# Kernel optimization log

Measured on AMD Instinct MI355X. Metric: run time of the kernel, lower is better.

Reference implementation:

```python
import jax, jax.numpy as jnp
import numpy as np

NUM_CLASSES = 256
N_ITERS = 25  # fixed Lloyd iterations (sklearn default max_iter=300; fixed count for a jit-able reference)


def setup_inputs() -> dict:
    key = jax.random.key(0)
    k1, k2 = jax.random.split(key)
    features = jax.random.normal(k1, (65536, 1024), dtype=jnp.float32)
    logits = jax.random.normal(k2, (65536, 256), dtype=jnp.float32)
    return {"features": features, "logits": logits}


def _segment_mean_centroids(features, labels, num_classes, prev_centroids):
    # scatter-mean of features into per-class centroids; keep previous centroid if a class is empty
    sums = jax.ops.segment_sum(features, labels, num_segments=num_classes)      # [C, D]
    counts = jax.ops.segment_sum(jnp.ones((features.shape[0],), features.dtype),
                                 labels, num_segments=num_classes)               # [C]
    has = counts > 0
    means = sums / jnp.maximum(counts, 1.0)[:, None]
    return jnp.where(has[:, None], means, prev_centroids)


def _assign(features, centroids):
    # argmin of squared euclidean distance; ||x||^2 term is constant per row, drop it
    # scores[n, c] = -2 x_n . mu_c + ||mu_c||^2
    scores = -2.0 * jnp.einsum('nd,cd->nc', features, centroids) + jnp.sum(centroids * centroids, axis=1)[None, :]
    return jnp.argmin(scores, axis=1)


def reference(features, logits):
    # KMeans.forward: labels = argmax(logits); centroids init from label centers (centroid_init='label_centers');
    # then Lloyd's k-means (sklearn KMeans with init=centroids, n_init=1) and return cluster labels.
    init_labels = jnp.argmax(logits, axis=1)
    # get_centroids: empty classes stay at zero
    zeros = jnp.zeros((NUM_CLASSES, features.shape[1]), features.dtype)
    centroids = _segment_mean_centroids(features, init_labels, NUM_CLASSES, zeros)

    def body(i, centroids):
        labels = _assign(features, centroids)
        return _segment_mean_centroids(features, labels, NUM_CLASSES, centroids)

    centroids = jax.lax.fori_loop(0, N_ITERS, body, centroids)
    pseudo_labels = _assign(features, centroids)
    return pseudo_labels.astype(jnp.int64)
```

## Files before the change

### kernel.cpp

```cpp
#include <hip/hip_runtime.h>

#define N_PTS 65536
#define DIM   1024
#define NCLS  256
#define NITER 25

typedef __attribute__((ext_vector_type(8)))  short short8;
typedef __attribute__((ext_vector_type(16))) float f32x16;

__device__ __forceinline__ unsigned short bf_split(float x, float& rem) {
    unsigned u = __float_as_uint(x);
    unsigned b = (u + 0x7fffu + ((u >> 16) & 1u)) & 0xffff0000u;
    rem = x - __uint_as_float(b);
    return (unsigned short)(b >> 16);
}
__device__ __forceinline__ unsigned short bf_rne(float x) {
    unsigned u = __float_as_uint(x);
    return (unsigned short)((u + 0x7fffu + ((u >> 16) & 1u)) >> 16);
}

__device__ __forceinline__ void gload_lds16(const void* g, void* l) {
    __builtin_amdgcn_global_load_lds(
        (const __attribute__((address_space(1))) unsigned int*)g,
        (__attribute__((address_space(3))) unsigned int*)l, 16, 0, 0);
}

__global__ void k_argmax(const float* __restrict__ logits, int* __restrict__ labels) {
    int row  = blockIdx.x * 4 + (threadIdx.x >> 6);
    int lane = threadIdx.x & 63;
    float4 v = reinterpret_cast<const float4*>(logits + (size_t)row * NCLS)[lane];
    float bv = v.x; int bi = lane * 4;
    if (v.y > bv) { bv = v.y; bi = lane * 4 + 1; }
    if (v.z > bv) { bv = v.z; bi = lane * 4 + 2; }
    if (v.w > bv) { bv = v.w; bi = lane * 4 + 3; }
    #pragma unroll
    for (int off = 32; off >= 1; off >>= 1) {
        float ov = __shfl_down(bv, off, 64);
        int   oi = __shfl_down(bi, off, 64);
        if (ov > bv || (ov == bv && oi < bi)) { bv = ov; bi = oi; }
    }
    if (lane == 0) labels[row] = bi;
}

__global__ void k_hist(const int* __restrict__ labels, int* __restrict__ counts) {
    __shared__ int h[NCLS];
    h[threadIdx.x] = 0;
    __syncthreads();
    for (int i = blockIdx.x * blockDim.x + threadIdx.x; i < N_PTS;
         i += gridDim.x * blockDim.x)
        atomicAdd(&h[labels[i]], 1);
    __syncthreads();
    int v = h[threadIdx.x];
    if (v) atomicAdd(&counts[threadIdx.x], v);
}

__global__ __launch_bounds__(512) void k_accum(const float* __restrict__ feat,
                                               const int* __restrict__ labels,
                                               float* __restrict__ partials) {
    __shared__ unsigned long long s[NCLS * 32];
    int tid = threadIdx.x;
    for (int i = tid; i < NCLS * 32; i += 512) s[i] = 0ull;
    __syncthreads();
    int slice = blockIdx.x;
    int chunk = blockIdx.y;
    int w = tid >> 6, l = tid & 63;
    int sub = l >> 3;
    int dq  = l & 7;
    const size_t dbase = (size_t)slice * 32 + dq * 4;
    for (int step = 0; step < 128; ++step) {
        int p = chunk * 8192 + step * 64 + w * 8 + sub;
        int c = labels[p];
        float4 f = *reinterpret_cast<const float4*>(feat + (size_t)p * DIM + dbase);
        unsigned long long* dst = &s[c * 32 + dq * 4];
        atomicAdd(dst + 0, (unsigned long long)__double2ll_rn((double)f.x * 16777216.0));
        atomicAdd(dst + 1, (unsigned long long)__double2ll_rn((double)f.y * 16777216.0));
        atomicAdd(dst + 2, (unsigned long long)__double2ll_rn((double)f.z * 16777216.0));
        atomicAdd(dst + 3, (unsigned long long)__double2ll_rn((double)f.w * 16777216.0));
    }
    __syncthreads();
    float* out = partials + (size_t)chunk * NCLS * DIM;
    for (int i = tid; i < NCLS * 32; i += 512) {
        int c = i >> 5, d = i & 31;
        out[(size_t)c * DIM + slice * 32 + d] =
            (float)((double)(long long)s[i] * (1.0 / 16777216.0));
    }
}

__global__ void k_finalize(const float* __restrict__ partials,
                           const int* __restrict__ counts,
                           float* __restrict__ centroids) {
    int idx = blockIdx.x * blockDim.x + threadIdx.x;
    int c = idx >> 8;
    size_t off = (size_t)idx * 4;
    float4 sum = make_float4(0.f, 0.f, 0.f, 0.f);
    for (int ch = 0; ch < 8; ++ch) {
        float4 p = *reinterpret_cast<const float4*>(partials + (size_t)ch * NCLS * DIM + off);
        sum.x += p.x; sum.y += p.y; sum.z += p.z; sum.w += p.w;
    }
    int cnt = counts[c];
    float4 outv;
    if (cnt > 0) {
        float fc = (float)cnt;
        outv = make_float4(sum.x / fc, sum.y / fc, sum.z / fc, sum.w / fc);
    } else {
        outv = *reinterpret_cast<const float4*>(centroids + off);
    }
    *reinterpret_cast<float4*>(centroids + off) = outv;
}

__global__ void k_norms(const float* __restrict__ centroids, float* __restrict__ norms) {
    int c = blockIdx.x;
    int t = threadIdx.x;
    float4 v = reinterpret_cast<const float4*>(centroids + (size_t)c * DIM)[t];
    float s = v.x * v.x + v.y * v.y + v.z * v.z + v.w * v.w;
    __shared__ float red[4];
    #pragma unroll
    for (int off = 32; off >= 1; off >>= 1) s += __shfl_down(s, off, 64);
    if ((t & 63) == 0) red[t >> 6] = s;
    __syncthreads();
    if (t == 0) norms[c] = red[0] + red[1] + red[2] + red[3];
}

__global__ void k_splitB(const float* __restrict__ cent, unsigned short* __restrict__ Bs) {
    int lin = blockIdx.x * 256 + threadIdx.x;
    int n = lin & 255, kg = lin >> 8;
    int k = kg * 8;
    int kc = kg >> 2, kh = (kg >> 1) & 1, jg = kg & 1;
    int nt = n >> 5, lane = (n & 31) + 32 * jg;
    const float* src = cent + (size_t)n * DIM + k;
    unsigned short hi[8], mi[8], lo[8];
    #pragma unroll
    for (int j = 0; j < 8; ++j) {
        float r1, r2;
        hi[j] = bf_split(src[j], r1);
        mi[j] = bf_split(r1, r2);
        lo[j] = bf_rne(r2);
    }
    #pragma unroll
    for (int p = 0; p < 3; ++p) {
        size_t base = ((((size_t)kc * 3 + p) * 8 + nt) * 2 + kh) * 512 + (size_t)lane * 8;
        const unsigned short* srcp = (p == 0) ? hi : (p == 1) ? mi : lo;
        uint4 pack = *reinterpret_cast<const uint4*>(srcp);
        *reinterpret_cast<uint4*>(Bs + base) = pack;
    }
}

__global__ __launch_bounds__(256, 3) void k_assign(
        const float* __restrict__ feat, const unsigned short* __restrict__ Bs,
        const float* __restrict__ norms, unsigned long long* __restrict__ part) {
    __shared__ __align__(16) unsigned short Bl[24 * 512];
    int tid = threadIdx.x, w = tid >> 6, l = tid & 63;
    int cn = l & 31, jg = l >> 5;
    int p0 = blockIdx.x * 128;
    int nh = blockIdx.y;
    int n0 = nh * 128;

    f32x16 acc[4];
    #pragma unroll
    for (int t = 0; t < 4; ++t)
        #pragma unroll
        for (int i = 0; i < 16; ++i) acc[t][i] = 0.f;

    const float* arow = feat + (size_t)(p0 + w * 32 + cn) * DIM + jg * 8;

    for (int kc = 0; kc < 32; ++kc) {
        int k0 = kc * 32;
        float4 g0 = *reinterpret_cast<const float4*>(arow + k0);
        float4 g1 = *reinterpret_cast<const float4*>(arow + k0 + 4);
        float4 g2 = *reinterpret_cast<const float4*>(arow + k0 + 16);
        float4 g3 = *reinterpret_cast<const float4*>(arow + k0 + 20);
        __syncthreads();
        #pragma unroll
        for (int i = 0; i < 6; ++i) {
            int s = w * 6 + i;
            int kh = s & 1, ntl = (s >> 1) & 3, q = s >> 3;
            int ntg = nh * 4 + ntl;
            const unsigned short* g =
                Bs + ((((size_t)kc * 3 + q) * 8 + ntg) * 2 + kh) * 512 + (size_t)l * 8;
            gload_lds16(g, &Bl[s * 512]);
        }
        float xs[16] = {g0.x, g0.y, g0.z, g0.w, g1.x, g1.y, g1.z, g1.w,
                        g2.x, g2.y, g2.z, g2.w, g3.x, g3.y, g3.z, g3.w};
        union { short8 v; unsigned short u[8]; } af[2][3];
        #pragma unroll
        for (int kh = 0; kh < 2; ++kh)
            #pragma unroll
            for (int j = 0; j < 8; ++j) {
                float r1, r2;
                af[kh][0].u[j] = bf_split(xs[kh * 8 + j], r1);
                af[kh][1].u[j] = bf_split(r1, r2);
                af[kh][2].u[j] = bf_rne(r2);
            }
        __syncthreads();
        #pragma unroll
        for (int q = 0; q < 3; ++q)
            #pragma unroll
            for (int ntl = 0; ntl < 4; ++ntl)
                #pragma unroll
                for (int kh = 0; kh < 2; ++kh) {
                    int s = (q * 4 + ntl) * 2 + kh;
                    short8 bf = *reinterpret_cast<const short8*>(&Bl[s * 512 + l * 8]);
                    acc[ntl] = __builtin_amdgcn_mfma_f32_32x32x16_bf16(
                        af[kh][0].v, bf, acc[ntl], 0, 0, 0);
                    if (q < 2)
                        acc[ntl] = __builtin_amdgcn_mfma_f32_32x32x16_bf16(
                            af[kh][1].v, bf, acc[ntl], 0, 0, 0);
                    if (q == 0)
                        acc[ntl] = __builtin_amdgcn_mfma_f32_32x32x16_bf16(
                            af[kh][2].v, bf, acc[ntl], 0, 0, 0);
                }
    }

    float nrm[4];
    #pragma unroll
    for (int ntl = 0; ntl < 4; ++ntl) nrm[ntl] = norms[n0 + ntl * 32 + cn];
    #pragma unroll
    for (int r = 0; r < 16; ++r) {
        unsigned long long key = ~0ull;
        #pragma unroll
        for (int ntl = 0; ntl < 4; ++ntl) {
            float s = nrm[ntl] - 2.0f * acc[ntl][r];
            unsigned u = __float_as_uint(s);
            u = (u & 0x80000000u) ? ~u : (u | 0x80000000u);
            unsigned long long kk =
                ((unsigned long long)u << 32) | (unsigned)(n0 + ntl * 32 + cn);
            key = (kk < key) ? kk : key;
        }
        #pragma unroll
        for (int off = 16; off >= 1; off >>= 1) {
            unsigned long long ok = __shfl_xor(key, off, 64);
            key = (ok < key) ? ok : key;
        }
        if (cn == 0) {
            int m = p0 + w * 32 + (r & 3) + 8 * (r >> 2) + 4 * jg;
            part[(size_t)nh * N_PTS + m] = key;
        }
    }
}

__global__ void k_combine(const unsigned long long* __restrict__ part,
                          int* __restrict__ labels) {
    int i = blockIdx.x * blockDim.x + threadIdx.x;
    unsigned long long a = part[i], b = part[N_PTS + i];
    unsigned long long k = (b < a) ? b : a;
    labels[i] = (int)(k & 0xffffffffull);
}

extern "C" void kernel_launch(void* const* d_in, const int* in_sizes, int n_in,
                              void* d_out, int out_size, void* d_ws, size_t ws_size,
                              hipStream_t stream) {
    const float* feat   = (const float*)d_in[0];
    const float* logits = (const float*)d_in[1];
    int* out_labels = (int*)d_out;

    char* ws = (char*)d_ws;
    float* centroids            = (float*)ws;
    float* partials             = (float*)(ws + 0x100000);
    float* norms                = (float*)(ws + 0x900000);
    int*   counts               = (int*)  (ws + 0x901000);
    int*   labels               = (int*)  (ws + 0x902000);
    unsigned short* Bs          = (unsigned short*)(ws + 0x950000);
    unsigned long long* part    = (unsigned long long*)(ws + 0xAD0000);

    k_argmax<<<N_PTS / 4, 256, 0, stream>>>(logits, labels);
    hipMemsetAsync(centroids, 0, (size_t)NCLS * DIM * sizeof(float), stream);
    hipMemsetAsync(counts, 0, NCLS * sizeof(int), stream);
    k_hist<<<64, 256, 0, stream>>>(labels, counts);
    k_accum<<<dim3(32, 8), 512, 0, stream>>>(feat, labels, partials);
    k_finalize<<<256, 256, 0, stream>>>(partials, counts, centroids);

    for (int it = 0; it < NITER; ++it) {
        k_norms<<<NCLS, 256, 0, stream>>>(centroids, norms);
        k_splitB<<<128, 256, 0, stream>>>(centroids, Bs);
        k_assign<<<dim3(N_PTS / 128, 2), 256, 0, stream>>>(feat, Bs, norms, part);
        k_combine<<<N_PTS / 256, 256, 0, stream>>>(part, labels);
        hipMemsetAsync(counts, 0, NCLS * sizeof(int), stream);
        k_hist<<<64, 256, 0, stream>>>(labels, counts);
        k_accum<<<dim3(32, 8), 512, 0, stream>>>(feat, labels, partials);
        k_finalize<<<256, 256, 0, stream>>>(partials, counts, centroids);
    }

    k_norms<<<NCLS, 256, 0, stream>>>(centroids, norms);
    k_splitB<<<128, 256, 0, stream>>>(centroids, Bs);
    k_assign<<<dim3(N_PTS / 128, 2), 256, 0, stream>>>(feat, Bs, norms, part);
    k_combine<<<N_PTS / 256, 256, 0, stream>>>(part, out_labels);
}
```

Measured before the change: 7.328 ms.

## Load B fragments directly to registers, prefetch A, fuse histogram into combine

The assign kernel drops its LDS staging of the split-bf16 centroid tiles. Each wave now reads its B fragments straight from global memory into registers, which removes both block barriers per K chunk. Feature loads for the next chunk are issued one iteration ahead to overlap with the MFMA work. Separately, the label histogram is folded into the combine kernel using shared-memory atomics, which removes the k_hist launch; the risks are redundant global and L2 traffic for B across waves and higher register pressure.

```diff
diff --git a/kernel.cpp b/kernel.cpp
--- a/kernel.cpp
+++ b/kernel.cpp
@@ -17,12 +17,6 @@
 __device__ __forceinline__ unsigned short bf_rne(float x) {
     unsigned u = __float_as_uint(x);
     return (unsigned short)((u + 0x7fffu + ((u >> 16) & 1u)) >> 16);
-}
-
-__device__ __forceinline__ void gload_lds16(const void* g, void* l) {
-    __builtin_amdgcn_global_load_lds(
-        (const __attribute__((address_space(1))) unsigned int*)g,
-        (__attribute__((address_space(3))) unsigned int*)l, 16, 0, 0);
 }
 
 __global__ void k_argmax(const float* __restrict__ logits, int* __restrict__ labels) {
@@ -148,7 +142,6 @@
 __global__ __launch_bounds__(256, 3) void k_assign(
         const float* __restrict__ feat, const unsigned short* __restrict__ Bs,
         const float* __restrict__ norms, unsigned long long* __restrict__ part) {
-    __shared__ __align__(16) unsigned short Bl[24 * 512];
     int tid = threadIdx.x, w = tid >> 6, l = tid & 63;
     int cn = l & 31, jg = l >> 5;
     int p0 = blockIdx.x * 128;
@@ -162,25 +155,23 @@
         for (int i = 0; i < 16; ++i) acc[t][i] = 0.f;
 
     const float* arow = feat + (size_t)(p0 + w * 32 + cn) * DIM + jg * 8;
+    const unsigned short* bbase = Bs + (size_t)nh * 4096 + (size_t)l * 8;
+
+    float4 ga0 = *reinterpret_cast<const float4*>(arow + 0);
+    float4 ga1 = *reinterpret_cast<const float4*>(arow + 4);
+    float4 ga2 = *reinterpret_cast<const float4*>(arow + 16);
+    float4 ga3 = *reinterpret_cast<const float4*>(arow + 20);
 
     for (int kc = 0; kc < 32; ++kc) {
-        int k0 = kc * 32;
-        float4 g0 = *reinterpret_cast<const float4*>(arow + k0);
-        float4 g1 = *reinterpret_cast<const float4*>(arow + k0 + 4);
-        float4 g2 = *reinterpret_cast<const float4*>(arow + k0 + 16);
-        float4 g3 = *reinterpret_cast<const float4*>(arow + k0 + 20);
-        __syncthreads();
-        #pragma unroll
-        for (int i = 0; i < 6; ++i) {
-            int s = w * 6 + i;
-            int kh = s & 1, ntl = (s >> 1) & 3, q = s >> 3;
-            int ntg = nh * 4 + ntl;
-            const unsigned short* g =
-                Bs + ((((size_t)kc * 3 + q) * 8 + ntg) * 2 + kh) * 512 + (size_t)l * 8;
-            gload_lds16(g, &Bl[s * 512]);
-        }
-        float xs[16] = {g0.x, g0.y, g0.z, g0.w, g1.x, g1.y, g1.z, g1.w,
-                        g2.x, g2.y, g2.z, g2.w, g3.x, g3.y, g3.z, g3.w};
+        float xs[16] = {ga0.x, ga0.y, ga0.z, ga0.w, ga1.x, ga1.y, ga1.z, ga1.w,
+                        ga2.x, ga2.y, ga2.z, ga2.w, ga3.x, ga3.y, ga3.z, ga3.w};
+        if (kc < 31) {
+            int k1 = (kc + 1) * 32;
+            ga0 = *reinterpret_cast<const float4*>(arow + k1);
+            ga1 = *reinterpret_cast<const float4*>(arow + k1 + 4);
+            ga2 = *reinterpret_cast<const float4*>(arow + k1 + 16);
+            ga3 = *reinterpret_cast<const float4*>(arow + k1 + 20);
+        }
         union { short8 v; unsigned short u[8]; } af[2][3];
         #pragma unroll
         for (int kh = 0; kh < 2; ++kh)
@@ -191,15 +182,21 @@
                 af[kh][1].u[j] = bf_split(r1, r2);
                 af[kh][2].u[j] = bf_rne(r2);
             }
-        __syncthreads();
-        #pragma unroll
-        for (int q = 0; q < 3; ++q)
+        const unsigned short* bkc = bbase + (size_t)kc * 24576;
+        #pragma unroll
+        for (int q = 0; q < 3; ++q) {
+            short8 bq[8];
+            #pragma unroll
+            for (int ntl = 0; ntl < 4; ++ntl)
+                #pragma unroll
+                for (int kh = 0; kh < 2; ++kh)
+                    bq[ntl * 2 + kh] = *reinterpret_cast<const short8*>(
+                        bkc + q * 8192 + ntl * 1024 + kh * 512);
             #pragma unroll
             for (int ntl = 0; ntl < 4; ++ntl)
                 #pragma unroll
                 for (int kh = 0; kh < 2; ++kh) {
-                    int s = (q * 4 + ntl) * 2 + kh;
-                    short8 bf = *reinterpret_cast<const short8*>(&Bl[s * 512 + l * 8]);
+                    short8 bf = bq[ntl * 2 + kh];
                     acc[ntl] = __builtin_amdgcn_mfma_f32_32x32x16_bf16(
                         af[kh][0].v, bf, acc[ntl], 0, 0, 0);
                     if (q < 2)
@@ -209,6 +206,7 @@
                         acc[ntl] = __builtin_amdgcn_mfma_f32_32x32x16_bf16(
                             af[kh][2].v, bf, acc[ntl], 0, 0, 0);
                 }
+        }
     }
 
     float nrm[4];
@@ -239,11 +237,19 @@
 }
 
 __global__ void k_combine(const unsigned long long* __restrict__ part,
-                          int* __restrict__ labels) {
-    int i = blockIdx.x * blockDim.x + threadIdx.x;
+                          int* __restrict__ labels, int* __restrict__ counts) {
+    __shared__ int h[NCLS];
+    h[threadIdx.x] = 0;
+    __syncthreads();
+    int i = blockIdx.x * 256 + threadIdx.x;
     unsigned long long a = part[i], b = part[N_PTS + i];
     unsigned long long k = (b < a) ? b : a;
-    labels[i] = (int)(k & 0xffffffffull);
+    int lab = (int)(k & 0xffffffffull);
+    labels[i] = lab;
+    atomicAdd(&h[lab], 1);
+    __syncthreads();
+    int v = h[threadIdx.x];
+    if (v) atomicAdd(&counts[threadIdx.x], v);
 }
 
 extern "C" void kernel_launch(void* const* d_in, const int* in_sizes, int n_in,
@@ -273,9 +279,8 @@
         k_norms<<<NCLS, 256, 0, stream>>>(centroids, norms);
         k_splitB<<<128, 256, 0, stream>>>(centroids, Bs);
         k_assign<<<dim3(N_PTS / 128, 2), 256, 0, stream>>>(feat, Bs, norms, part);
-        k_combine<<<N_PTS / 256, 256, 0, stream>>>(part, labels);
         hipMemsetAsync(counts, 0, NCLS * sizeof(int), stream);
-        k_hist<<<64, 256, 0, stream>>>(labels, counts);
+        k_combine<<<N_PTS / 256, 256, 0, stream>>>(part, labels, counts);
         k_accum<<<dim3(32, 8), 512, 0, stream>>>(feat, labels, partials);
         k_finalize<<<256, 256, 0, stream>>>(partials, counts, centroids);
     }
@@ -283,5 +288,6 @@
     k_norms<<<NCLS, 256, 0, stream>>>(centroids, norms);
     k_splitB<<<128, 256, 0, stream>>>(centroids, Bs);
     k_assign<<<dim3(N_PTS / 128, 2), 256, 0, stream>>>(feat, Bs, norms, part);
-    k_combine<<<N_PTS / 256, 256, 0, stream>>>(part, out_labels);
-}
+    hipMemsetAsync(counts, 0, NCLS * sizeof(int), stream);
+    k_combine<<<N_PTS / 256, 256, 0, stream>>>(part, out_labels, counts);
+}
```

Measured after the change: 8.541 ms. 16.6% more time.
